# Performance work log

Hardware: AMD Instinct MI355X
Metric: run time of the kernel (lower is better)

The kernel has to match this reference:

```python
import jax, jax.numpy as jnp
import numpy as np

B, S, E, H = 2, 2048, 1024, 16
D = E // H  # head size = 64


def setup_inputs() -> dict:
    key = jax.random.key(0)
    ks = jax.random.split(key, 13)
    scale = 1.0 / np.sqrt(E)
    inp = {
        "q": jax.random.normal(ks[0], (B, S, E), jnp.float32),
        "k": jax.random.normal(ks[1], (B, S, E), jnp.float32),
        "v": jax.random.normal(ks[2], (B, S, E), jnp.float32),
        "mask": jax.random.randint(ks[3], (B, 1, S, S), 0, 2, jnp.int32),
        "Wq": jax.random.normal(ks[4], (E, E), jnp.float32) * scale,
        "bq": jnp.zeros((E,), jnp.float32),
        "Wk": jax.random.normal(ks[5], (E, E), jnp.float32) * scale,
        "bk": jnp.zeros((E,), jnp.float32),
        "Wv": jax.random.normal(ks[6], (E, E), jnp.float32) * scale,
        "bv": jnp.zeros((E,), jnp.float32),
        "Wo": jax.random.normal(ks[7], (E, E), jnp.float32) * scale,
        "bo": jnp.zeros((E,), jnp.float32),
    }
    return inp


def reference(q, k, v, mask, Wq, bq, Wk, bk, Wv, bv, Wo, bo):
    # Linear projections (torch Linear: x @ W.T + b)
    qh = (q @ Wq.T + bq).reshape(B, S, H, D).transpose(0, 2, 1, 3)  # [B,H,S,D]
    kh = (k @ Wk.T + bk).reshape(B, S, H, D).transpose(0, 2, 1, 3)
    vh = (v @ Wv.T + bv).reshape(B, S, H, D).transpose(0, 2, 1, 3)

    scores = jnp.einsum("bhqd,bhkd->bhqk", qh, kh) / jnp.sqrt(jnp.float32(D))
    scores = jnp.where(mask == 0, jnp.float32(-1e10), scores)
    attn = jax.nn.softmax(scores, axis=-1)  # [B,H,S,S]
    ctx = jnp.einsum("bhqk,bhkd->bhqd", attn, vh)  # dropout p=0.0 -> identity

    out = ctx.transpose(0, 2, 1, 3).reshape(B, S, E)
    return out @ Wo.T + bo
```

## Files before the change

kernel.cpp:

```cpp
#include <hip/hip_runtime.h>

typedef unsigned short ushort_t;
typedef __attribute__((ext_vector_type(8))) short short8;
typedef __attribute__((ext_vector_type(4))) float f32x4;
typedef __attribute__((ext_vector_type(4))) unsigned short ushort4_t;
typedef __attribute__((ext_vector_type(4))) unsigned int uint4_t;

#define BB 2
#define SS 2048
#define EE 1024
#define HH 16
#define DD 64
#define MM (BB*SS)

#define QB_OFF  0u
#define KB_OFF  4194304u
#define VB_OFF  8388608u
#define WQ_OFF  12582912u
#define WK_OFF  13631488u
#define WV_OFF  14680064u
#define WO_OFF  15728640u
#define QH_OFF  16777216u
#define KH_OFF  20971520u
#define VT_OFF  25165824u
#define CTX_OFF QB_OFF
#define MB_OFF  29360128u

__device__ __forceinline__ ushort_t f2bf(float x) {
    unsigned u = __builtin_bit_cast(unsigned, x);
    u += 0x7FFFu + ((u >> 16) & 1u);
    return (ushort_t)(u >> 16);
}

__device__ __forceinline__ unsigned pk_bf16(float a, float b) {
    unsigned ua = __builtin_bit_cast(unsigned, a);
    unsigned ub = __builtin_bit_cast(unsigned, b);
    ua += 0x7FFFu + ((ua >> 16) & 1u);
    ub += 0x7FFFu + ((ub >> 16) & 1u);
    return __builtin_amdgcn_perm(ub, ua, 0x07060302u);
}

__device__ __forceinline__ void load_lds16(const void* g, void* l) {
    __builtin_amdgcn_global_load_lds((const __attribute__((address_space(1))) void*)g,
                                     (__attribute__((address_space(3))) void*)l, 16, 0, 0);
}

__global__ __launch_bounds__(256) void prep_kernel(
    const float* __restrict__ q, const float* __restrict__ k, const float* __restrict__ v,
    const int* __restrict__ mask,
    const float* __restrict__ Wq, const float* __restrict__ Wk,
    const float* __restrict__ Wv, const float* __restrict__ Wo,
    ushort_t* __restrict__ wsb, unsigned* __restrict__ maskbits)
{
    int g = blockIdx.x;
    if (g < 16384) {
        int idx = g * 256 + threadIdx.x;
        const float* src; ushort_t* dst; int rel;
        if      (idx < 1048576) { src = q;  dst = wsb + QB_OFF; rel = idx; }
        else if (idx < 2097152) { src = k;  dst = wsb + KB_OFF; rel = idx - 1048576; }
        else if (idx < 3145728) { src = v;  dst = wsb + VB_OFF; rel = idx - 2097152; }
        else if (idx < 3407872) { src = Wq; dst = wsb + WQ_OFF; rel = idx - 3145728; }
        else if (idx < 3670016) { src = Wk; dst = wsb + WK_OFF; rel = idx - 3407872; }
        else if (idx < 3932160) { src = Wv; dst = wsb + WV_OFF; rel = idx - 3670016; }
        else                    { src = Wo; dst = wsb + WO_OFF; rel = idx - 3932160; }
        f32x4 val = ((const f32x4*)src)[rel];
        ushort4_t o;
        o.x = f2bf(val.x); o.y = f2bf(val.y); o.z = f2bf(val.z); o.w = f2bf(val.w);
        ((ushort4_t*)dst)[rel] = o;
    } else {
        int t = (g - 16384) * 256 + threadIdx.x;
        int b   = t >> 17;
        int rem = t & 131071;
        int w   = rem >> 11;
        int sk  = rem & 2047;
        unsigned bits = 0;
        const int* mp = mask + ((size_t)b * SS + (size_t)w * 32) * SS + sk;
        #pragma unroll
        for (int jj = 0; jj < 32; ++jj)
            bits |= (mp[(size_t)jj * SS] != 0 ? 1u : 0u) << jj;
        maskbits[((size_t)b * SS + sk) * 64 + w] = bits;
    }
}

__device__ __forceinline__ void gemm_mainloop(
    const ushort_t* __restrict__ A, const ushort_t* __restrict__ Bm,
    int m0, int n0, f32x4 acc[4][4], ushort_t* As, ushort_t* Bs)
{
    const int tid  = threadIdx.x;
    const int wave = tid >> 6, lane = tid & 63;
    const int r16  = lane >> 2;
    const int c8   = (lane & 3) * 8;
    const int lane15 = lane & 15, quad = lane >> 4;
    const int wm = wave >> 1, wn = wave & 1;

    #pragma unroll 1
    for (int kt = 0; kt < 32; ++kt) {
        const int k0 = kt * 32;
        __syncthreads();
        const ushort_t* ga = A  + (size_t)(m0 + wave * 32 + r16) * 1024 + k0 + c8;
        load_lds16(ga,             As + wave * 1024);
        load_lds16(ga + 16 * 1024, As + wave * 1024 + 512);
        const ushort_t* gb = Bm + (size_t)(n0 + wave * 32 + r16) * 1024 + k0 + c8;
        load_lds16(gb,             Bs + wave * 1024);
        load_lds16(gb + 16 * 1024, Bs + wave * 1024 + 512);
        __syncthreads();

        short8 a[4], bf[4];
        #pragma unroll
        for (int i = 0; i < 4; ++i)
            a[i] = *(const short8*)&As[(wm * 64 + i * 16 + lane15) * 32 + quad * 8];
        #pragma unroll
        for (int j = 0; j < 4; ++j)
            bf[j] = *(const short8*)&Bs[(wn * 64 + j * 16 + lane15) * 32 + quad * 8];
        #pragma unroll
        for (int i = 0; i < 4; ++i)
            #pragma unroll
            for (int j = 0; j < 4; ++j)
                acc[i][j] = __builtin_amdgcn_mfma_f32_16x16x32_bf16(a[i], bf[j], acc[i][j], 0, 0, 0);
    }
}

__global__ __launch_bounds__(256) void gemm_qkv(
    ushort_t* __restrict__ wsb,
    const float* __restrict__ bq, const float* __restrict__ bk, const float* __restrict__ bv)
{
    __shared__ ushort_t As[128 * 32], Bs[128 * 32];
    const int z = blockIdx.z;
    const ushort_t* A  = wsb + (z == 0 ? QB_OFF : z == 1 ? KB_OFF : VB_OFF);
    const ushort_t* Bm = wsb + (z == 0 ? WQ_OFF : z == 1 ? WK_OFF : WV_OFF);
    const float* bias  = (z == 0) ? bq : (z == 1) ? bk : bv;
    ushort_t* dst      = wsb + (z == 0 ? QH_OFF : z == 1 ? KH_OFF : VT_OFF);
    const int m0 = blockIdx.y * 128, n0 = blockIdx.x * 128;

    f32x4 acc[4][4];
    #pragma unroll
    for (int i = 0; i < 4; ++i)
        #pragma unroll
        for (int j = 0; j < 4; ++j) acc[i][j] = (f32x4){0.f, 0.f, 0.f, 0.f};

    gemm_mainloop(A, Bm, m0, n0, acc, As, Bs);

    const int tid = threadIdx.x, wave = tid >> 6, lane = tid & 63;
    const int lane15 = lane & 15, quad = lane >> 4;
    const int wm = wave >> 1, wn = wave & 1;
    const float scale = (z == 0) ? 0.180336880111f : 1.0f;

    #pragma unroll
    for (int i = 0; i < 4; ++i) {
        #pragma unroll
        for (int j = 0; j < 4; ++j) {
            int col = n0 + wn * 64 + j * 16 + lane15;
            float bv_ = bias[col];
            int hh = col >> 6, d = col & 63;
            #pragma unroll
            for (int r = 0; r < 4; ++r) {
                int row = m0 + wm * 64 + i * 16 + quad * 4 + r;
                int bb = row >> 11, s = row & 2047;
                float val = (acc[i][j][r] + bv_) * scale;
                size_t off;
                if (z < 2) {
                    off = (((size_t)bb * HH + hh) * SS + s) * DD + d;
                } else {
                    int kk = s & 127;
                    int sp = (s & ~127) + ((kk & 15) << 3) + (kk >> 4);
                    off = (((size_t)bb * HH + hh) * DD + d) * SS + sp;
                }
                dst[off] = f2bf(val);
            }
        }
    }
}

__global__ __launch_bounds__(256, 2) void attn_kernel(
    const ushort_t* __restrict__ wsb, const unsigned* __restrict__ maskbits,
    ushort_t* __restrict__ ctx)
{
    __shared__ ushort_t Ks[128 * 64];
    __shared__ ushort_t Vts[64 * 128];
    __shared__ ushort_t Ps[128 * 128];

    const int tid  = threadIdx.x;
    const int wave = tid >> 6, lane = tid & 63;
    const int lane15 = lane & 15, quad = lane >> 4;
    const int sw7 = lane15 & 7;
    const int bh = blockIdx.y;
    const int b  = bh >> 4, h = bh & 15;
    const int q0 = blockIdx.x * 128;

    const ushort_t* Qh  = wsb + QH_OFF;
    const ushort_t* Kh  = wsb + KH_OFF;
    const ushort_t* VhT = wsb + VT_OFF;

    short8 qfrag[2][2];
    #pragma unroll
    for (int i = 0; i < 2; ++i)
        #pragma unroll
        for (int ks = 0; ks < 2; ++ks)
            qfrag[i][ks] = *(const short8*)(Qh +
                ((size_t)bh * SS + q0 + wave * 32 + i * 16 + lane15) * DD + ks * 32 + quad * 8);

    short8 ones_frag;
    {
        short onev = (lane15 == 0) ? (short)0x3F80 : (short)0;
        #pragma unroll
        for (int e = 0; e < 8; ++e) ones_frag[e] = onev;
    }

    const f32x4 zero4 = (f32x4){0.f, 0.f, 0.f, 0.f};
    f32x4 s_acc[2][8];
    f32x4 o_acc[2][4];
    f32x4 osum[2];
    #pragma unroll
    for (int i = 0; i < 2; ++i) {
        #pragma unroll
        for (int jd = 0; jd < 4; ++jd) o_acc[i][jd] = zero4;
        osum[i] = zero4;
    }

    #pragma unroll 1
    for (int kt = 0; kt < 16; ++kt) {
        const int k0 = kt * 128;
        __syncthreads();

        const ushort_t* Kbase = Kh + ((size_t)bh * SS + k0) * DD;
        #pragma unroll
        for (int cc = 0; cc < 4; ++cc) {
            int n = (wave * 4 + cc) * 64 + lane;
            int row = n >> 3;
            int c = (n & 7) ^ (row & 7);
            load_lds16(Kbase + row * 64 + c * 8, Ks + (wave * 4 + cc) * 512);
        }
        const ushort_t* Vbase = VhT + ((size_t)bh * DD) * SS + k0;
        #pragma unroll
        for (int cc = 0; cc < 4; ++cc) {
            int n = (wave * 4 + cc) * 64 + lane;
            int d = n >> 4;
            int c = (n & 15) ^ (d & 7);
            load_lds16(Vbase + (size_t)d * SS + c * 8, Vts + (wave * 4 + cc) * 512);
        }

        unsigned mw[8];
        {
            const int qw = (q0 >> 5) + wave;
            #pragma unroll
            for (int j = 0; j < 8; ++j) {
                int sk = k0 + j * 16 + lane15;
                mw[j] = maskbits[((size_t)b * SS + sk) * 64 + qw];
            }
        }
        __syncthreads();

        #pragma unroll
        for (int j = 0; j < 8; ++j) {
            short8 bf = *(const short8*)&Ks[(j * 16 + lane15) * 64 + ((quad ^ sw7) << 3)];
            s_acc[0][j] = __builtin_amdgcn_mfma_f32_16x16x32_bf16(qfrag[0][0], bf, zero4, 0, 0, 0);
            s_acc[1][j] = __builtin_amdgcn_mfma_f32_16x16x32_bf16(qfrag[1][0], bf, zero4, 0, 0, 0);
        }
        #pragma unroll
        for (int j = 0; j < 8; ++j) {
            short8 bf = *(const short8*)&Ks[(j * 16 + lane15) * 64 + (((4 + quad) ^ sw7) << 3)];
            s_acc[0][j] = __builtin_amdgcn_mfma_f32_16x16x32_bf16(qfrag[0][1], bf, s_acc[0][j], 0, 0, 0);
            s_acc[1][j] = __builtin_amdgcn_mfma_f32_16x16x32_bf16(qfrag[1][1], bf, s_acc[1][j], 0, 0, 0);
        }

        #pragma unroll
        for (int i = 0; i < 2; ++i) {
            #pragma unroll
            for (int r = 0; r < 4; ++r) {
                const int bit = i * 16 + quad * 4 + r;
                float p[8];
                #pragma unroll
                for (int j = 0; j < 8; ++j) {
                    float e = __builtin_amdgcn_exp2f(s_acc[i][j][r]);
                    p[j] = ((mw[j] >> bit) & 1u) ? e : 0.f;
                }
                uint4_t pk;
                pk.x = pk_bf16(p[0], p[1]);
                pk.y = pk_bf16(p[2], p[3]);
                pk.z = pk_bf16(p[4], p[5]);
                pk.w = pk_bf16(p[6], p[7]);
                const int row = wave * 32 + i * 16 + quad * 4 + r;
                *(uint4_t*)&Ps[row * 128 + ((lane15 ^ (row & 7)) << 3)] = pk;
            }
        }

        #pragma unroll
        for (int kb = 0; kb < 4; ++kb) {
            short8 ap[2];
            #pragma unroll
            for (int i = 0; i < 2; ++i)
                ap[i] = *(const short8*)&Ps[(wave * 32 + i * 16 + lane15) * 128 +
                                            (((kb * 4 + quad) ^ sw7) << 3)];
            #pragma unroll
            for (int jd = 0; jd < 4; ++jd) {
                short8 bv_ = *(const short8*)&Vts[(jd * 16 + lane15) * 128 +
                                                  (((kb * 4 + quad) ^ sw7) << 3)];
                o_acc[0][jd] = __builtin_amdgcn_mfma_f32_16x16x32_bf16(ap[0], bv_, o_acc[0][jd], 0, 0, 0);
                o_acc[1][jd] = __builtin_amdgcn_mfma_f32_16x16x32_bf16(ap[1], bv_, o_acc[1][jd], 0, 0, 0);
            }
            osum[0] = __builtin_amdgcn_mfma_f32_16x16x32_bf16(ap[0], ones_frag, osum[0], 0, 0, 0);
            osum[1] = __builtin_amdgcn_mfma_f32_16x16x32_bf16(ap[1], ones_frag, osum[1], 0, 0, 0);
        }
    }

    #pragma unroll
    for (int i = 0; i < 2; ++i) {
        #pragma unroll
        for (int r = 0; r < 4; ++r) {
            float l = __shfl(osum[i][r], lane & 48);
            float inv = 1.0f / l;
            int row = q0 + wave * 32 + i * 16 + quad * 4 + r;
            #pragma unroll
            for (int jd = 0; jd < 4; ++jd) {
                int col = h * DD + jd * 16 + lane15;
                ctx[((size_t)b * SS + row) * EE + col] = f2bf(o_acc[i][jd][r] * inv);
            }
        }
    }
}

__global__ __launch_bounds__(256) void gemm_out(
    const ushort_t* __restrict__ wsb, const float* __restrict__ bo, float* __restrict__ out)
{
    __shared__ ushort_t As[128 * 32], Bs[128 * 32];
    const ushort_t* A  = wsb + CTX_OFF;
    const ushort_t* Bm = wsb + WO_OFF;
    const int m0 = blockIdx.y * 128, n0 = blockIdx.x * 128;

    f32x4 acc[4][4];
    #pragma unroll
    for (int i = 0; i < 4; ++i)
        #pragma unroll
        for (int j = 0; j < 4; ++j) acc[i][j] = (f32x4){0.f, 0.f, 0.f, 0.f};

    gemm_mainloop(A, Bm, m0, n0, acc, As, Bs);

    const int tid = threadIdx.x, wave = tid >> 6, lane = tid & 63;
    const int lane15 = lane & 15, quad = lane >> 4;
    const int wm = wave >> 1, wn = wave & 1;

    #pragma unroll
    for (int i = 0; i < 4; ++i) {
        #pragma unroll
        for (int j = 0; j < 4; ++j) {
            int col = n0 + wn * 64 + j * 16 + lane15;
            float bv_ = bo[col];
            #pragma unroll
            for (int r = 0; r < 4; ++r) {
                int row = m0 + wm * 64 + i * 16 + quad * 4 + r;
                out[(size_t)row * EE + col] = acc[i][j][r] + bv_;
            }
        }
    }
}

extern "C" void kernel_launch(void* const* d_in, const int* in_sizes, int n_in,
                              void* d_out, int out_size, void* d_ws, size_t ws_size,
                              hipStream_t stream) {
    const float* q    = (const float*)d_in[0];
    const float* k    = (const float*)d_in[1];
    const float* v    = (const float*)d_in[2];
    const int*   mask = (const int*)  d_in[3];
    const float* Wq   = (const float*)d_in[4];
    const float* bq   = (const float*)d_in[5];
    const float* Wk   = (const float*)d_in[6];
    const float* bk   = (const float*)d_in[7];
    const float* Wv   = (const float*)d_in[8];
    const float* bv   = (const float*)d_in[9];
    const float* Wo   = (const float*)d_in[10];
    const float* bo   = (const float*)d_in[11];

    ushort_t* wsb = (ushort_t*)d_ws;
    unsigned* maskbits = (unsigned*)(wsb + MB_OFF);

    prep_kernel<<<17408, 256, 0, stream>>>(q, k, v, mask, Wq, Wk, Wv, Wo, wsb, maskbits);
    gemm_qkv<<<dim3(8, 32, 3), 256, 0, stream>>>(wsb, bq, bk, bv);
    attn_kernel<<<dim3(16, 32), 256, 0, stream>>>(wsb, maskbits, wsb + CTX_OFF);
    gemm_out<<<dim3(8, 32), 256, 0, stream>>>(wsb, bo, (float*)d_out);
}
```

Baseline: 304.9 us.

## Compute V projection transposed for contiguous stores; shrink out-proj tiles

For the V projection, the GEMM operands are swapped so the block computes Wv·Vᵀ directly. The transposed V layout can then be written with lanes writing along the sequence dimension instead of scattered strided stores. The bias is indexed per row in this path. Separately, the output projection uses 64x128 tiles with each wave owning 16 rows, which doubles the grid to 512 blocks for better CU occupancy, at the cost of lower per-block reuse and a sync per 32-wide k step.

```diff
diff --git a/kernel.cpp b/kernel.cpp
--- a/kernel.cpp
+++ b/kernel.cpp
@@ -126,11 +126,15 @@
 {
     __shared__ ushort_t As[128 * 32], Bs[128 * 32];
     const int z = blockIdx.z;
-    const ushort_t* A  = wsb + (z == 0 ? QB_OFF : z == 1 ? KB_OFF : VB_OFF);
-    const ushort_t* Bm = wsb + (z == 0 ? WQ_OFF : z == 1 ? WK_OFF : WV_OFF);
+    const ushort_t* A;
+    const ushort_t* Bm;
+    if      (z == 0) { A = wsb + QB_OFF; Bm = wsb + WQ_OFF; }
+    else if (z == 1) { A = wsb + KB_OFF; Bm = wsb + WK_OFF; }
+    else             { A = wsb + WV_OFF; Bm = wsb + VB_OFF; }
     const float* bias  = (z == 0) ? bq : (z == 1) ? bk : bv;
     ushort_t* dst      = wsb + (z == 0 ? QH_OFF : z == 1 ? KH_OFF : VT_OFF);
-    const int m0 = blockIdx.y * 128, n0 = blockIdx.x * 128;
+    const int m0 = (z < 2) ? blockIdx.y * 128 : blockIdx.x * 128;
+    const int n0 = (z < 2) ? blockIdx.x * 128 : blockIdx.y * 128;
 
     f32x4 acc[4][4];
     #pragma unroll
@@ -145,27 +149,40 @@
     const int wm = wave >> 1, wn = wave & 1;
     const float scale = (z == 0) ? 0.180336880111f : 1.0f;
 
-    #pragma unroll
-    for (int i = 0; i < 4; ++i) {
-        #pragma unroll
-        for (int j = 0; j < 4; ++j) {
-            int col = n0 + wn * 64 + j * 16 + lane15;
-            float bv_ = bias[col];
-            int hh = col >> 6, d = col & 63;
+    if (z < 2) {
+        #pragma unroll
+        for (int i = 0; i < 4; ++i) {
+            #pragma unroll
+            for (int j = 0; j < 4; ++j) {
+                int col = n0 + wn * 64 + j * 16 + lane15;
+                float bv_ = bias[col];
+                int hh = col >> 6, d = col & 63;
+                #pragma unroll
+                for (int r = 0; r < 4; ++r) {
+                    int row = m0 + wm * 64 + i * 16 + quad * 4 + r;
+                    int bb = row >> 11, s = row & 2047;
+                    float val = (acc[i][j][r] + bv_) * scale;
+                    dst[(((size_t)bb * HH + hh) * SS + s) * DD + d] = f2bf(val);
+                }
+            }
+        }
+    } else {
+        #pragma unroll
+        for (int i = 0; i < 4; ++i) {
             #pragma unroll
             for (int r = 0; r < 4; ++r) {
                 int row = m0 + wm * 64 + i * 16 + quad * 4 + r;
-                int bb = row >> 11, s = row & 2047;
-                float val = (acc[i][j][r] + bv_) * scale;
-                size_t off;
-                if (z < 2) {
-                    off = (((size_t)bb * HH + hh) * SS + s) * DD + d;
-                } else {
+                float bv_ = bias[row];
+                int hh = row >> 6, d = row & 63;
+                #pragma unroll
+                for (int j = 0; j < 4; ++j) {
+                    int col = n0 + wn * 64 + j * 16 + lane15;
+                    int bb = col >> 11, s = col & 2047;
                     int kk = s & 127;
-                    int sp = (s & ~127) + ((kk & 15) << 3) + (kk >> 4);
-                    off = (((size_t)bb * HH + hh) * DD + d) * SS + sp;
+                    int sp = ((kk & 15) << 3) + (kk >> 4);
+                    dst[(((size_t)bb * HH + hh) * DD + d) * SS + (s & ~127) + sp]
+                        = f2bf(acc[i][j][r] + bv_);
                 }
-                dst[off] = f2bf(val);
             }
         }
     }
@@ -322,34 +339,52 @@
 __global__ __launch_bounds__(256) void gemm_out(
     const ushort_t* __restrict__ wsb, const float* __restrict__ bo, float* __restrict__ out)
 {
-    __shared__ ushort_t As[128 * 32], Bs[128 * 32];
+    __shared__ ushort_t As[64 * 32];
+    __shared__ ushort_t Bs[128 * 32];
     const ushort_t* A  = wsb + CTX_OFF;
     const ushort_t* Bm = wsb + WO_OFF;
-    const int m0 = blockIdx.y * 128, n0 = blockIdx.x * 128;
-
-    f32x4 acc[4][4];
-    #pragma unroll
-    for (int i = 0; i < 4; ++i)
-        #pragma unroll
-        for (int j = 0; j < 4; ++j) acc[i][j] = (f32x4){0.f, 0.f, 0.f, 0.f};
-
-    gemm_mainloop(A, Bm, m0, n0, acc, As, Bs);
+    const int m0 = blockIdx.y * 64, n0 = blockIdx.x * 128;
 
     const int tid = threadIdx.x, wave = tid >> 6, lane = tid & 63;
     const int lane15 = lane & 15, quad = lane >> 4;
-    const int wm = wave >> 1, wn = wave & 1;
-
-    #pragma unroll
-    for (int i = 0; i < 4; ++i) {
-        #pragma unroll
-        for (int j = 0; j < 4; ++j) {
-            int col = n0 + wn * 64 + j * 16 + lane15;
-            float bv_ = bo[col];
-            #pragma unroll
-            for (int r = 0; r < 4; ++r) {
-                int row = m0 + wm * 64 + i * 16 + quad * 4 + r;
-                out[(size_t)row * EE + col] = acc[i][j][r] + bv_;
-            }
+
+    f32x4 acc[8];
+    #pragma unroll
+    for (int j = 0; j < 8; ++j) acc[j] = (f32x4){0.f, 0.f, 0.f, 0.f};
+
+    #pragma unroll 1
+    for (int kt = 0; kt < 32; ++kt) {
+        const int k0 = kt * 32;
+        __syncthreads();
+        {
+            int n = wave * 64 + lane;
+            load_lds16(A + (size_t)(m0 + (n >> 2)) * 1024 + k0 + (n & 3) * 8,
+                       As + wave * 512);
+        }
+        #pragma unroll
+        for (int m = 0; m < 2; ++m) {
+            int n = m * 256 + wave * 64 + lane;
+            load_lds16(Bm + (size_t)(n0 + (n >> 2)) * 1024 + k0 + (n & 3) * 8,
+                       Bs + (m * 256 + wave * 64) * 8);
+        }
+        __syncthreads();
+
+        short8 a = *(const short8*)&As[(wave * 16 + lane15) * 32 + quad * 8];
+        #pragma unroll
+        for (int j = 0; j < 8; ++j) {
+            short8 bf = *(const short8*)&Bs[(j * 16 + lane15) * 32 + quad * 8];
+            acc[j] = __builtin_amdgcn_mfma_f32_16x16x32_bf16(a, bf, acc[j], 0, 0, 0);
+        }
+    }
+
+    #pragma unroll
+    for (int j = 0; j < 8; ++j) {
+        int col = n0 + j * 16 + lane15;
+        float bv_ = bo[col];
+        #pragma unroll
+        for (int r = 0; r < 4; ++r) {
+            int row = m0 + wave * 16 + quad * 4 + r;
+            out[(size_t)row * EE + col] = acc[j][r] + bv_;
         }
     }
 }
@@ -376,5 +411,5 @@
     prep_kernel<<<17408, 256, 0, stream>>>(q, k, v, mask, Wq, Wk, Wv, Wo, wsb, maskbits);
     gemm_qkv<<<dim3(8, 32, 3), 256, 0, stream>>>(wsb, bq, bk, bv);
     attn_kernel<<<dim3(16, 32), 256, 0, stream>>>(wsb, maskbits, wsb + CTX_OFF);
-    gemm_out<<<dim3(8, 32), 256, 0, stream>>>(wsb, bo, (float*)d_out);
-}
+    gemm_out<<<dim3(8, 64), 256, 0, stream>>>(wsb, bo, (float*)d_out);
+}
```

New measurement: 291.9 us. 1.04x faster.
